# Kernel optimization log

Hardware: AMD Instinct MI355X
Metric: run time of the kernel (lower is better)

## Reference

```python
import jax, jax.numpy as jnp
import numpy as np

THR = 1.0   # snntorch Leaky default threshold
BETA = 0.9  # leak factor from the module


@jax.custom_vjp
def atan_spike(x):
    # Heaviside forward; ATan surrogate gradient (snntorch default alpha=2):
    # d/dx = 1 / (1 + (pi * x)^2)
    return (x > 0).astype(x.dtype)

def _atan_fwd(x):
    return (x > 0).astype(x.dtype), x

def _atan_bwd(x, g):
    return (g / (1.0 + (jnp.pi * x) ** 2),)

atan_spike.defvjp(_atan_fwd, _atan_bwd)


def setup_inputs() -> dict:
    key = jax.random.key(0)
    k0, k1, k2, k3, k4 = jax.random.split(key, 5)
    B, T, L = 256, 1000, 30  # 24 = L - 7 + 1 matches fc1 in_features 16*24
    out_c = 35
    x = jax.random.normal(k0, (B, T, L), dtype=jnp.float32)
    conv_w = jax.random.normal(k1, (16, 1, 7), dtype=jnp.float32) / np.float32(np.sqrt(7.0))
    conv_b = jax.random.normal(k2, (16,), dtype=jnp.float32) * 0.05
    fc_w = jax.random.normal(k3, (out_c, 16 * 24), dtype=jnp.float32) / np.float32(np.sqrt(384.0))
    fc_b = jax.random.normal(k4, (out_c,), dtype=jnp.float32) * 0.05
    return {"x": x, "conv_w": conv_w, "conv_b": conv_b, "fc_w": fc_w, "fc_b": fc_b}


def reference(x, conv_w, conv_b, fc_w, fc_b):
    B, T, L = x.shape
    # Conv1d has no recurrence -> hoist it out of the time loop, batched over B*T.
    cur1 = jax.lax.conv_general_dilated(
        x.reshape(B * T, 1, L), conv_w, window_strides=(1,), padding="VALID",
        dimension_numbers=("NCH", "OIH", "NCH"),
    ) + conv_b[None, :, None]                      # (B*T, 16, 24)
    Lo = cur1.shape[-1]
    cur1 = cur1.reshape(B, T, 16, Lo).transpose(1, 0, 2, 3)  # (T, B, 16, 24)
    out_c = fc_w.shape[0]

    def step(carry, c1):
        mem1, mem2 = carry
        # LIF1: reset-by-subtraction using detached spike of previous membrane
        r1 = jax.lax.stop_gradient((mem1 > THR).astype(mem1.dtype))
        mem1 = BETA * mem1 + c1 - r1 * THR
        spk1 = atan_spike(mem1 - THR)              # (B, 16, 24)
        c2 = spk1.reshape(B, 16 * Lo) @ fc_w.T + fc_b  # (B, out_c)
        # LIF2
        r2 = jax.lax.stop_gradient((mem2 > THR).astype(mem2.dtype))
        mem2 = BETA * mem2 + c2 - r2 * THR
        return (mem1, mem2), mem2

    init = (jnp.zeros((B, 16, Lo), x.dtype), jnp.zeros((B, out_c), x.dtype))
    _, mem2_rec = jax.lax.scan(step, init, cur1)   # (T, B, out_c)
    return mem2_rec.mean(axis=0)                   # (B, out_c)
```

## Files before the change

### kernel.cpp

```cpp
#include <hip/hip_runtime.h>

typedef _Float16 half8 __attribute__((ext_vector_type(8)));
typedef float f32x4 __attribute__((ext_vector_type(4)));

#define SPH  32
#define NIT  34
#define SPKW 392
#define XTW  36
#define C2W  48
#define TN   1000

__global__ __launch_bounds__(1024, 4) void snn_fwd(
    const float* __restrict__ x,
    const float* __restrict__ conv_w,
    const float* __restrict__ conv_b,
    const float* __restrict__ fc_w,
    const float* __restrict__ fc_b,
    float* __restrict__ out)
{
    __shared__ __align__(16) _Float16 spk[2][SPH][SPKW];
    __shared__ __align__(16) float    xsT[2][30][XTW];
    __shared__ __align__(16) float    c2L[2][SPH][C2W];

    const int tid  = threadIdx.x;
    const int b    = blockIdx.x;
    const int wid  = tid >> 6;
    const int lane = tid & 63;

    const int ct = tid;
    const int c  = ct & 15;
    const int p  = ct >> 4;
    float wk[7];
    float cb = 0.f;
    if (wid < 6) {
#pragma unroll
        for (int k = 0; k < 7; ++k) wk[k] = conv_w[c * 7 + k];
        cb = conv_b[c];
    }

    const int g  = wid - 6;
    const int m  = g >> 1;
    const int tb = g & 1;
    const int nL = lane & 15;
    const int q  = lane >> 4;
    half8 A[12];
    if (wid >= 6 && wid < 12) {
        const int o = m * 16 + nL;
#pragma unroll
        for (int kt = 0; kt < 12; ++kt) {
            half8 a;
#pragma unroll
            for (int j = 0; j < 8; ++j) {
                int Kp = kt * 32 + q * 8 + j;
                int Kc = Kp & 15;
                int Kq = Kp >> 4;
                a[j] = (o < 35) ? (_Float16)fc_w[o * 384 + Kc * 24 + Kq]
                                : (_Float16)0.f;
            }
            A[kt] = a;
        }
    }

    const int st4 = tid - 768;
    int fs[4], fl[4];
    if (wid >= 12) {
#pragma unroll
        for (int r = 0; r < 4; ++r) {
            int f = st4 + 256 * r;
            fs[r] = f / 30;
            fl[r] = f % 30;
        }
    }
    const float fcb = (wid == 12 && lane < 35) ? fc_b[lane] : 0.f;

    float m1 = 0.f, sp = 0.f;
    float mem2 = 0.f, accO = 0.f;
    float xr[4];

    const float* xb = x + (size_t)b * (TN * 30);

    if (wid >= 12) {
#pragma unroll
        for (int r = 0; r < 4; ++r) {
            int f = st4 + 256 * r;
            if (f < 960) xsT[0][fl[r]][fs[r]] = xb[f];
        }
#pragma unroll
        for (int r = 0; r < 4; ++r) {
            int f = st4 + 256 * r;
            xr[r] = (f < 960) ? xb[960 + f] : 0.f;
        }
    }
    __syncthreads();

#pragma unroll 1
    for (int ph = 0; ph < NIT; ++ph) {
        if (wid < 6) {
            if (ph < 32) {
                const float* xcol = &xsT[ph & 1][p][0];
                unsigned short* sdst = (unsigned short*)&spk[ph & 1][0][ct];
#pragma unroll 2
                for (int s0 = 0; s0 < SPH; s0 += 4) {
                    f32x4 xv[7];
#pragma unroll
                    for (int k = 0; k < 7; ++k)
                        xv[k] = *(const f32x4*)(xcol + k * XTW + s0);
                    float cc[4];
#pragma unroll
                    for (int dt = 0; dt < 4; ++dt) cc[dt] = cb;
#pragma unroll
                    for (int k = 0; k < 7; ++k) {
#pragma unroll
                        for (int dt = 0; dt < 4; ++dt)
                            cc[dt] = fmaf(wk[k], xv[k][dt], cc[dt]);
                    }
#pragma unroll
                    for (int dt = 0; dt < 4; ++dt) {
                        m1 = fmaf(0.9f, m1, cc[dt] - sp);
                        sp = (m1 > 1.0f) ? 1.0f : 0.0f;
                        sdst[(s0 + dt) * SPKW] =
                            (m1 > 1.0f) ? (unsigned short)0x3C00u : (unsigned short)0u;
                    }
                }
            }
        } else if (wid < 12) {
            if (ph >= 1 && ph <= 32) {
                const _Float16* sb = &spk[(ph - 1) & 1][0][0];
                half8 B[12];
#pragma unroll
                for (int kt = 0; kt < 12; ++kt)
                    B[kt] = *(const half8*)(sb + (tb * 16 + nL) * SPKW + kt * 32 + q * 8);
                f32x4 acc = {0.f, 0.f, 0.f, 0.f};
#pragma unroll
                for (int kt = 0; kt < 12; ++kt)
                    acc = __builtin_amdgcn_mfma_f32_16x16x32_f16(A[kt], B[kt], acc, 0, 0, 0);
                float* cd = &c2L[(ph - 1) & 1][0][0];
                *(f32x4*)(cd + (tb * 16 + nL) * C2W + m * 16 + q * 4) = acc;
            }
        } else {
            if (ph <= 30) {
                float* dst = &xsT[(ph + 1) & 1][0][0];
#pragma unroll
                for (int r = 0; r < 4; ++r) {
                    int f = st4 + 256 * r;
                    if (f < 960) dst[fl[r] * XTW + fs[r]] = xr[r];
                }
            }
            if (ph <= 29) {
                const float* src = xb + (size_t)(ph + 2) * (SPH * 30);
#pragma unroll
                for (int r = 0; r < 4; ++r) {
                    int f = st4 + 256 * r;
                    int t = (ph + 2) * SPH + fs[r];
                    xr[r] = (f < 960 && t < TN) ? src[f] : 0.f;
                }
            }
            if (wid == 12 && lane < 35 && ph >= 2) {
                const float* cs = &c2L[(ph - 2) & 1][0][0];
                float v[SPH];
#pragma unroll
                for (int j = 0; j < SPH; ++j) v[j] = cs[j * C2W + lane];
                const int tbase = (ph - 2) * SPH;
#pragma unroll
                for (int j = 0; j < SPH; ++j) {
                    float r2 = (mem2 > 1.0f) ? 1.0f : 0.0f;
                    mem2 = 0.9f * mem2 + (v[j] + fcb) - r2;
                    if (tbase + j < TN) accO += mem2;
                }
            }
        }
        __syncthreads();
    }

    if (wid == 12 && lane < 35) out[b * 35 + lane] = accO * (1.0f / (float)TN);
}

extern "C" void kernel_launch(void* const* d_in, const int* in_sizes, int n_in,
                              void* d_out, int out_size, void* d_ws, size_t ws_size,
                              hipStream_t stream) {
    const float* x      = (const float*)d_in[0];
    const float* conv_w = (const float*)d_in[1];
    const float* conv_b = (const float*)d_in[2];
    const float* fc_w   = (const float*)d_in[3];
    const float* fc_b   = (const float*)d_in[4];
    float* out          = (float*)d_out;

    snn_fwd<<<256, 1024, 0, stream>>>(x, conv_w, conv_b, fc_w, fc_b, out);
}
```

Baseline: 146.5 us.

## Shrink block to 576 threads by merging warp roles and pairing conv channels

The block drops from 16 to 9 wavefronts. Each conv/LIF1 thread now handles two channels and writes both spike halves as one packed 32-bit store. The separate loader wavefronts are gone, and the six MFMA wavefronts now also stage global x into shared memory and run the LIF2 recurrence. The aim is to cut idle wavefronts and barrier cost, and to give each conv thread more independent work. In exchange, the MFMA wavefronts take on extra load and store work on the critical path, and each conv thread carries a longer serial chain.

```diff
diff --git a/kernel.cpp b/kernel.cpp
--- a/kernel.cpp
+++ b/kernel.cpp
@@ -10,7 +10,7 @@
 #define C2W  48
 #define TN   1000
 
-__global__ __launch_bounds__(1024, 4) void snn_fwd(
+__global__ __launch_bounds__(576, 1) void snn_fwd(
     const float* __restrict__ x,
     const float* __restrict__ conv_w,
     const float* __restrict__ conv_b,
@@ -27,24 +27,29 @@
     const int wid  = tid >> 6;
     const int lane = tid & 63;
 
-    const int ct = tid;
-    const int c  = ct & 15;
-    const int p  = ct >> 4;
-    float wk[7];
-    float cb = 0.f;
-    if (wid < 6) {
-#pragma unroll
-        for (int k = 0; k < 7; ++k) wk[k] = conv_w[c * 7 + k];
-        cb = conv_b[c];
-    }
-
-    const int g  = wid - 6;
+    const int ct    = tid;
+    const int cpair = ct & 7;
+    const int p     = ct >> 3;
+    const int c0    = cpair * 2;
+    float wk0[7], wk1[7];
+    float cb0 = 0.f, cb1 = 0.f;
+    if (wid < 3) {
+#pragma unroll
+        for (int k = 0; k < 7; ++k) {
+            wk0[k] = conv_w[c0 * 7 + k];
+            wk1[k] = conv_w[(c0 + 1) * 7 + k];
+        }
+        cb0 = conv_b[c0];
+        cb1 = conv_b[c0 + 1];
+    }
+
+    const int g  = wid - 3;
     const int m  = g >> 1;
     const int tb = g & 1;
     const int nL = lane & 15;
     const int q  = lane >> 4;
     half8 A[12];
-    if (wid >= 6 && wid < 12) {
+    if (wid >= 3) {
         const int o = m * 16 + nL;
 #pragma unroll
         for (int kt = 0; kt < 12; ++kt) {
@@ -60,34 +65,35 @@
             A[kt] = a;
         }
     }
-
-    const int st4 = tid - 768;
-    int fs[4], fl[4];
-    if (wid >= 12) {
-#pragma unroll
-        for (int r = 0; r < 4; ++r) {
-            int f = st4 + 256 * r;
+    const float fcb = (wid == 3 && lane < 35) ? fc_b[lane] : 0.f;
+
+    const int st = tid - 192;
+    int fs[3], fl[3];
+    if (wid >= 3) {
+#pragma unroll
+        for (int r = 0; r < 3; ++r) {
+            int f = st + 384 * r;
             fs[r] = f / 30;
             fl[r] = f % 30;
         }
     }
-    const float fcb = (wid == 12 && lane < 35) ? fc_b[lane] : 0.f;
-
-    float m1 = 0.f, sp = 0.f;
+
+    float m1a = 0.f, spa = 0.f;
+    float m1b = 0.f, spb = 0.f;
     float mem2 = 0.f, accO = 0.f;
-    float xr[4];
+    float xr[3];
 
     const float* xb = x + (size_t)b * (TN * 30);
 
-    if (wid >= 12) {
-#pragma unroll
-        for (int r = 0; r < 4; ++r) {
-            int f = st4 + 256 * r;
+    if (wid >= 3) {
+#pragma unroll
+        for (int r = 0; r < 3; ++r) {
+            int f = st + 384 * r;
             if (f < 960) xsT[0][fl[r]][fs[r]] = xb[f];
         }
 #pragma unroll
-        for (int r = 0; r < 4; ++r) {
-            int f = st4 + 256 * r;
+        for (int r = 0; r < 3; ++r) {
+            int f = st + 384 * r;
             xr[r] = (f < 960) ? xb[960 + f] : 0.f;
         }
     }
@@ -95,35 +101,52 @@
 
 #pragma unroll 1
     for (int ph = 0; ph < NIT; ++ph) {
-        if (wid < 6) {
+        if (wid < 3) {
             if (ph < 32) {
                 const float* xcol = &xsT[ph & 1][p][0];
-                unsigned short* sdst = (unsigned short*)&spk[ph & 1][0][ct];
+                unsigned int* sdst =
+                    (unsigned int*)&spk[ph & 1][0][p * 16 + c0];
 #pragma unroll 2
                 for (int s0 = 0; s0 < SPH; s0 += 4) {
                     f32x4 xv[7];
 #pragma unroll
                     for (int k = 0; k < 7; ++k)
                         xv[k] = *(const f32x4*)(xcol + k * XTW + s0);
-                    float cc[4];
-#pragma unroll
-                    for (int dt = 0; dt < 4; ++dt) cc[dt] = cb;
+                    float ca[4], cc[4];
+#pragma unroll
+                    for (int dt = 0; dt < 4; ++dt) { ca[dt] = cb0; cc[dt] = cb1; }
 #pragma unroll
                     for (int k = 0; k < 7; ++k) {
 #pragma unroll
-                        for (int dt = 0; dt < 4; ++dt)
-                            cc[dt] = fmaf(wk[k], xv[k][dt], cc[dt]);
+                        for (int dt = 0; dt < 4; ++dt) {
+                            ca[dt] = fmaf(wk0[k], xv[k][dt], ca[dt]);
+                            cc[dt] = fmaf(wk1[k], xv[k][dt], cc[dt]);
+                        }
                     }
 #pragma unroll
                     for (int dt = 0; dt < 4; ++dt) {
-                        m1 = fmaf(0.9f, m1, cc[dt] - sp);
-                        sp = (m1 > 1.0f) ? 1.0f : 0.0f;
-                        sdst[(s0 + dt) * SPKW] =
-                            (m1 > 1.0f) ? (unsigned short)0x3C00u : (unsigned short)0u;
+                        m1a = fmaf(0.9f, m1a, ca[dt] - spa);
+                        spa = (m1a > 1.0f) ? 1.0f : 0.0f;
+                        m1b = fmaf(0.9f, m1b, cc[dt] - spb);
+                        spb = (m1b > 1.0f) ? 1.0f : 0.0f;
+                        unsigned int pk = (m1a > 1.0f ? 0x00003C00u : 0u) |
+                                          (m1b > 1.0f ? 0x3C000000u : 0u);
+                        sdst[(s0 + dt) * (SPKW / 2)] = pk;
                     }
                 }
             }
-        } else if (wid < 12) {
+        } else {
+            const bool ldg = (ph <= 29);
+            float xn[3];
+            if (ldg) {
+                const float* src = xb + (size_t)(ph + 2) * (SPH * 30);
+#pragma unroll
+                for (int r = 0; r < 3; ++r) {
+                    int f = st + 384 * r;
+                    int t = (ph + 2) * SPH + fs[r];
+                    xn[r] = (f < 960 && t < TN) ? src[f] : 0.f;
+                }
+            }
             if (ph >= 1 && ph <= 32) {
                 const _Float16* sb = &spk[(ph - 1) & 1][0][0];
                 half8 B[12];
@@ -137,25 +160,7 @@
                 float* cd = &c2L[(ph - 1) & 1][0][0];
                 *(f32x4*)(cd + (tb * 16 + nL) * C2W + m * 16 + q * 4) = acc;
             }
-        } else {
-            if (ph <= 30) {
-                float* dst = &xsT[(ph + 1) & 1][0][0];
-#pragma unroll
-                for (int r = 0; r < 4; ++r) {
-                    int f = st4 + 256 * r;
-                    if (f < 960) dst[fl[r] * XTW + fs[r]] = xr[r];
-                }
-            }
-            if (ph <= 29) {
-                const float* src = xb + (size_t)(ph + 2) * (SPH * 30);
-#pragma unroll
-                for (int r = 0; r < 4; ++r) {
-                    int f = st4 + 256 * r;
-                    int t = (ph + 2) * SPH + fs[r];
-                    xr[r] = (f < 960 && t < TN) ? src[f] : 0.f;
-                }
-            }
-            if (wid == 12 && lane < 35 && ph >= 2) {
+            if (wid == 3 && lane < 35 && ph >= 2) {
                 const float* cs = &c2L[(ph - 2) & 1][0][0];
                 float v[SPH];
 #pragma unroll
@@ -168,11 +173,23 @@
                     if (tbase + j < TN) accO += mem2;
                 }
             }
+            if (ph <= 30) {
+                float* dst = &xsT[(ph + 1) & 1][0][0];
+#pragma unroll
+                for (int r = 0; r < 3; ++r) {
+                    int f = st + 384 * r;
+                    if (f < 960) dst[fl[r] * XTW + fs[r]] = xr[r];
+                }
+            }
+            if (ldg) {
+#pragma unroll
+                for (int r = 0; r < 3; ++r) xr[r] = xn[r];
+            }
         }
         __syncthreads();
     }
 
-    if (wid == 12 && lane < 35) out[b * 35 + lane] = accO * (1.0f / (float)TN);
+    if (wid == 3 && lane < 35) out[b * 35 + lane] = accO * (1.0f / (float)TN);
 }
 
 extern "C" void kernel_launch(void* const* d_in, const int* in_sizes, int n_in,
@@ -185,5 +202,5 @@
     const float* fc_b   = (const float*)d_in[4];
     float* out          = (float*)d_out;
 
-    snn_fwd<<<256, 1024, 0, stream>>>(x, conv_w, conv_b, fc_w, fc_b, out);
+    snn_fwd<<<256, 576, 0, stream>>>(x, conv_w, conv_b, fc_w, fc_b, out);
 }
```

Measured after the change: 150.2 us. 2.5% more time.
